# Optimization experiments

Hardware: AMD Instinct MI355X
Metric: run time of the kernel (lower is better)

The kernel has to match this reference:

```python
import jax, jax.numpy as jnp
import numpy as np

B, H, W, C, G = 64, 32, 32, 512, 1024


def setup_inputs() -> dict:
    key = jax.random.key(0)
    k1, k2, k3, k4 = jax.random.split(key, 4)
    lcf = jax.random.normal(k1, (B, H, W, C), dtype=jnp.float32)
    gbf = jax.random.normal(k2, (B, G), dtype=jnp.float32)
    # Dense(C, use_bias=False) applied to G-dim input -> kernel [G, C]
    W_proj = jax.random.normal(k3, (G, C), dtype=jnp.float32) * (G ** -0.5)
    # Dense(1, use_bias=False) applied to C-dim input -> kernel [C, 1]
    W_pc = jax.random.normal(k4, (C, 1), dtype=jnp.float32) * (C ** -0.5)
    return {"lcf": lcf, "gbf": gbf, "W_proj": W_proj, "W_pc": W_pc}


def reference(lcf, gbf, W_proj, W_pc):
    # project global feature G -> C (glf_channel != lcf_channel path)
    gbf_pj = gbf @ W_proj                              # [B, C]
    lcf_rs = lcf.reshape(-1, H * W, C)                 # [B, N, C], N = H*W
    # 'pc' (parametrised compatibility): score = (lcf + gbf) @ W_pc
    add = lcf_rs + gbf_pj[:, None, :]                  # [B, N, C]
    c = jnp.squeeze(add @ W_pc, -1)                    # [B, N]
    a = jax.nn.softmax(c, axis=1)                      # softmax over spatial locations
    # weighted sum of local features: ga[b,c] = sum_n lcf_rs[b,n,c] * a[b,n]
    ga = jnp.einsum('bnc,bn->bc', lcf_rs, a)           # [B, C]
    return ga, a.reshape(-1, H, W)
```

## Files before the change

### kernel.cpp

```cpp
#include <hip/hip_runtime.h>

#define Bb 64
#define Cc 512
#define Gg 1024
#define Nn 1024
#define NCHUNK 16
#define CHUNK (Nn / NCHUNK)

__global__ void k_wv(const float* __restrict__ Wp, const float* __restrict__ Wpc,
                     float* __restrict__ wv) {
    int wave = (blockIdx.x * blockDim.x + threadIdx.x) >> 6;
    int lane = threadIdx.x & 63;
    if (wave >= Gg) return;
    const float4* row = (const float4*)(Wp + (size_t)wave * Cc);
    const float4* pc  = (const float4*)Wpc;
    float4 a0 = row[lane * 2], a1 = row[lane * 2 + 1];
    float4 b0 = pc[lane * 2],  b1 = pc[lane * 2 + 1];
    float s = a0.x*b0.x + a0.y*b0.y + a0.z*b0.z + a0.w*b0.w
            + a1.x*b1.x + a1.y*b1.y + a1.z*b1.z + a1.w*b1.w;
    for (int off = 32; off; off >>= 1) s += __shfl_down(s, off);
    if (lane == 0) wv[wave] = s;
}

__global__ void k_bias(const float* __restrict__ gbf, const float* __restrict__ wv,
                       float* __restrict__ bias) {
    int wave = (blockIdx.x * blockDim.x + threadIdx.x) >> 6;
    int lane = threadIdx.x & 63;
    if (wave >= Bb) return;
    const float4* g4 = (const float4*)(gbf + (size_t)wave * Gg);
    const float4* w4 = (const float4*)wv;
    float s = 0.f;
    #pragma unroll
    for (int i = 0; i < 4; ++i) {
        float4 a = g4[lane * 4 + i], b = w4[lane * 4 + i];
        s += a.x*b.x + a.y*b.y + a.z*b.z + a.w*b.w;
    }
    for (int off = 32; off; off >>= 1) s += __shfl_down(s, off);
    if (lane == 0) bias[wave] = s;
}

__global__ void k_score(const float* __restrict__ lcf, const float* __restrict__ Wpc,
                        const float* __restrict__ bias, float* __restrict__ score) {
    int row  = (blockIdx.x * blockDim.x + threadIdx.x) >> 6;
    int lane = threadIdx.x & 63;
    const float4* r4 = (const float4*)(lcf + (size_t)row * Cc);
    const float4* pc = (const float4*)Wpc;
    float4 a0 = r4[lane * 2], a1 = r4[lane * 2 + 1];
    float4 b0 = pc[lane * 2], b1 = pc[lane * 2 + 1];
    float s = a0.x*b0.x + a0.y*b0.y + a0.z*b0.z + a0.w*b0.w
            + a1.x*b1.x + a1.y*b1.y + a1.z*b1.z + a1.w*b1.w;
    for (int off = 32; off; off >>= 1) s += __shfl_down(s, off);
    if (lane == 0) score[row] = s + bias[row >> 10];
}

__global__ void k_softmax(float* __restrict__ sc) {
    int b = blockIdx.x;
    int t = threadIdx.x;
    int lane = t & 63, wid = t >> 6;
    __shared__ float red[16];
    float v = sc[b * Nn + t];

    float m = v;
    for (int off = 32; off; off >>= 1) m = fmaxf(m, __shfl_down(m, off));
    if (lane == 0) red[wid] = m;
    __syncthreads();
    if (wid == 0) {
        float mm = (lane < 16) ? red[lane] : -INFINITY;
        for (int off = 32; off; off >>= 1) mm = fmaxf(mm, __shfl_down(mm, off));
        if (lane == 0) red[0] = mm;
    }
    __syncthreads();
    m = red[0];
    __syncthreads();

    float e = expf(v - m);
    float s = e;
    for (int off = 32; off; off >>= 1) s += __shfl_down(s, off);
    if (lane == 0) red[wid] = s;
    __syncthreads();
    if (wid == 0) {
        float ss = (lane < 16) ? red[lane] : 0.f;
        for (int off = 32; off; off >>= 1) ss += __shfl_down(ss, off);
        if (lane == 0) red[0] = ss;
    }
    __syncthreads();
    s = red[0];

    sc[b * Nn + t] = e / s;
}

__global__ void k_wsum(const float* __restrict__ lcf, const float* __restrict__ prob,
                       float* __restrict__ ga) {
    int b  = blockIdx.x >> 4;
    int ch = blockIdx.x & (NCHUNK - 1);
    int t  = threadIdx.x;
    __shared__ float aw[CHUNK];
    if (t < CHUNK) aw[t] = prob[b * Nn + ch * CHUNK + t];
    __syncthreads();
    const float2* base = (const float2*)(lcf + ((size_t)(b * Nn + ch * CHUNK)) * Cc);
    float2 acc = {0.f, 0.f};
    #pragma unroll 4
    for (int n = 0; n < CHUNK; ++n) {
        float2 v = base[(size_t)n * (Cc / 2) + t];
        float w = aw[n];
        acc.x += v.x * w;
        acc.y += v.y * w;
    }
    atomicAdd(&ga[b * Cc + 2 * t],     acc.x);
    atomicAdd(&ga[b * Cc + 2 * t + 1], acc.y);
}

extern "C" void kernel_launch(void* const* d_in, const int* in_sizes, int n_in,
                              void* d_out, int out_size, void* d_ws, size_t ws_size,
                              hipStream_t stream) {
    const float* lcf = (const float*)d_in[0];
    const float* gbf = (const float*)d_in[1];
    const float* Wp  = (const float*)d_in[2];
    const float* Wpc = (const float*)d_in[3];

    float* out = (float*)d_out;
    float* ga  = out;
    float* a   = out + Bb * Cc;

    float* wv   = (float*)d_ws;
    float* bias = wv + Gg;

    hipMemsetAsync(ga, 0, Bb * Cc * sizeof(float), stream);

    k_wv     <<<Gg / 4,        256, 0, stream>>>(Wp, Wpc, wv);
    k_bias   <<<Bb / 4,        256, 0, stream>>>(gbf, wv, bias);
    k_score  <<<(Bb * Nn) / 4, 256, 0, stream>>>(lcf, Wpc, bias, a);
    k_softmax<<<Bb,           1024, 0, stream>>>(a);
    k_wsum   <<<Bb * NCHUNK,   256, 0, stream>>>(lcf, a, ga);
}
```

Before: 218.7 us.

## Fuse score, online softmax and weighted sum into single pass over features

Replaces five kernels with a flash-style fused kernel that computes scores, running max/sum and rescaled weighted feature sums per 16-row partition in one read of the local features, followed by a small combine kernel that merges partitions and writes normalized attention and outputs. The global-feature projection bias is dropped since it is constant per batch and cancels in the softmax. This removes the second full pass over the large feature tensor, the memset and the atomics, at the cost of a partial-sum workspace and serial per-row shuffle reductions.

```diff
diff --git a/kernel.cpp b/kernel.cpp
--- a/kernel.cpp
+++ b/kernel.cpp
@@ -2,134 +2,122 @@
 
 #define Bb 64
 #define Cc 512
-#define Gg 1024
 #define Nn 1024
-#define NCHUNK 16
-#define CHUNK (Nn / NCHUNK)
+#define NCH 16
+#define CHUNK 64
+#define RPW 16
+#define NPART 64
 
-__global__ void k_wv(const float* __restrict__ Wp, const float* __restrict__ Wpc,
-                     float* __restrict__ wv) {
-    int wave = (blockIdx.x * blockDim.x + threadIdx.x) >> 6;
-    int lane = threadIdx.x & 63;
-    if (wave >= Gg) return;
-    const float4* row = (const float4*)(Wp + (size_t)wave * Cc);
-    const float4* pc  = (const float4*)Wpc;
-    float4 a0 = row[lane * 2], a1 = row[lane * 2 + 1];
-    float4 b0 = pc[lane * 2],  b1 = pc[lane * 2 + 1];
-    float s = a0.x*b0.x + a0.y*b0.y + a0.z*b0.z + a0.w*b0.w
-            + a1.x*b1.x + a1.y*b1.y + a1.z*b1.z + a1.w*b1.w;
-    for (int off = 32; off; off >>= 1) s += __shfl_down(s, off);
-    if (lane == 0) wv[wave] = s;
+__global__ __launch_bounds__(256) void k_flash(const float* __restrict__ lcf,
+                                               const float* __restrict__ Wpc,
+                                               float* __restrict__ c_raw,
+                                               float* __restrict__ mz,
+                                               float* __restrict__ S) {
+    int b    = blockIdx.x >> 4;
+    int ch   = blockIdx.x & 15;
+    int t    = threadIdx.x;
+    int w    = t >> 6;
+    int lane = t & 63;
+    int part = ch * 4 + w;
+
+    const float4* pc = (const float4*)Wpc;
+    float4 p0 = pc[lane * 2], p1 = pc[lane * 2 + 1];
+
+    int row0 = ch * CHUNK + w * RPW;
+    const float* base = lcf + ((size_t)b * Nn + row0) * Cc;
+
+    float m = -INFINITY, Z = 0.f;
+    float4 s0 = {0.f, 0.f, 0.f, 0.f}, s1 = {0.f, 0.f, 0.f, 0.f};
+    float myscore = 0.f;
+
+    for (int r = 0; r < RPW; ++r) {
+        const float4* row4 = (const float4*)(base + (size_t)r * Cc);
+        float4 v0 = row4[lane * 2], v1 = row4[lane * 2 + 1];
+        float d = v0.x*p0.x + v0.y*p0.y + v0.z*p0.z + v0.w*p0.w
+                + v1.x*p1.x + v1.y*p1.y + v1.z*p1.z + v1.w*p1.w;
+        #pragma unroll
+        for (int off = 32; off; off >>= 1) d += __shfl_xor(d, off);
+        if (lane == r) myscore = d;
+        float mn   = fmaxf(m, d);
+        float corr = __expf(m - mn);
+        float wgt  = __expf(d - mn);
+        Z = Z * corr + wgt;
+        s0.x = s0.x*corr + wgt*v0.x;  s0.y = s0.y*corr + wgt*v0.y;
+        s0.z = s0.z*corr + wgt*v0.z;  s0.w = s0.w*corr + wgt*v0.w;
+        s1.x = s1.x*corr + wgt*v1.x;  s1.y = s1.y*corr + wgt*v1.y;
+        s1.z = s1.z*corr + wgt*v1.z;  s1.w = s1.w*corr + wgt*v1.w;
+        m = mn;
+    }
+
+    if (lane < RPW) c_raw[(size_t)b * Nn + row0 + lane] = myscore;
+    if (lane == 0) {
+        mz[((size_t)b * NPART + part) * 2]     = m;
+        mz[((size_t)b * NPART + part) * 2 + 1] = Z;
+    }
+    float4* Sp = (float4*)(S + ((size_t)b * NPART + part) * Cc);
+    Sp[lane * 2]     = s0;
+    Sp[lane * 2 + 1] = s1;
 }
 
-__global__ void k_bias(const float* __restrict__ gbf, const float* __restrict__ wv,
-                       float* __restrict__ bias) {
-    int wave = (blockIdx.x * blockDim.x + threadIdx.x) >> 6;
-    int lane = threadIdx.x & 63;
-    if (wave >= Bb) return;
-    const float4* g4 = (const float4*)(gbf + (size_t)wave * Gg);
-    const float4* w4 = (const float4*)wv;
-    float s = 0.f;
-    #pragma unroll
-    for (int i = 0; i < 4; ++i) {
-        float4 a = g4[lane * 4 + i], b = w4[lane * 4 + i];
-        s += a.x*b.x + a.y*b.y + a.z*b.z + a.w*b.w;
-    }
-    for (int off = 32; off; off >>= 1) s += __shfl_down(s, off);
-    if (lane == 0) bias[wave] = s;
-}
-
-__global__ void k_score(const float* __restrict__ lcf, const float* __restrict__ Wpc,
-                        const float* __restrict__ bias, float* __restrict__ score) {
-    int row  = (blockIdx.x * blockDim.x + threadIdx.x) >> 6;
-    int lane = threadIdx.x & 63;
-    const float4* r4 = (const float4*)(lcf + (size_t)row * Cc);
-    const float4* pc = (const float4*)Wpc;
-    float4 a0 = r4[lane * 2], a1 = r4[lane * 2 + 1];
-    float4 b0 = pc[lane * 2], b1 = pc[lane * 2 + 1];
-    float s = a0.x*b0.x + a0.y*b0.y + a0.z*b0.z + a0.w*b0.w
-            + a1.x*b1.x + a1.y*b1.y + a1.z*b1.z + a1.w*b1.w;
-    for (int off = 32; off; off >>= 1) s += __shfl_down(s, off);
-    if (lane == 0) score[row] = s + bias[row >> 10];
-}
-
-__global__ void k_softmax(float* __restrict__ sc) {
+__global__ __launch_bounds__(256) void k_combine(const float* __restrict__ c_raw,
+                                                 const float* __restrict__ mz,
+                                                 const float* __restrict__ S,
+                                                 float* __restrict__ ga,
+                                                 float* __restrict__ a) {
     int b = blockIdx.x;
     int t = threadIdx.x;
-    int lane = t & 63, wid = t >> 6;
-    __shared__ float red[16];
-    float v = sc[b * Nn + t];
+    __shared__ float lw[NPART];
+    __shared__ float sh_M, sh_invZ;
 
-    float m = v;
-    for (int off = 32; off; off >>= 1) m = fmaxf(m, __shfl_down(m, off));
-    if (lane == 0) red[wid] = m;
-    __syncthreads();
-    if (wid == 0) {
-        float mm = (lane < 16) ? red[lane] : -INFINITY;
-        for (int off = 32; off; off >>= 1) mm = fmaxf(mm, __shfl_down(mm, off));
-        if (lane == 0) red[0] = mm;
+    if (t < NPART) {
+        float mi = mz[((size_t)b * NPART + t) * 2];
+        float zi = mz[((size_t)b * NPART + t) * 2 + 1];
+        float M = mi;
+        #pragma unroll
+        for (int off = 32; off; off >>= 1) M = fmaxf(M, __shfl_xor(M, off));
+        float wi = __expf(mi - M);
+        float zc = zi * wi;
+        #pragma unroll
+        for (int off = 32; off; off >>= 1) zc += __shfl_xor(zc, off);
+        lw[t] = wi;
+        if (t == 0) { sh_M = M; sh_invZ = 1.f / zc; }
     }
     __syncthreads();
-    m = red[0];
-    __syncthreads();
+    float M = sh_M, invZ = sh_invZ;
 
-    float e = expf(v - m);
-    float s = e;
-    for (int off = 32; off; off >>= 1) s += __shfl_down(s, off);
-    if (lane == 0) red[wid] = s;
-    __syncthreads();
-    if (wid == 0) {
-        float ss = (lane < 16) ? red[lane] : 0.f;
-        for (int off = 32; off; off >>= 1) ss += __shfl_down(ss, off);
-        if (lane == 0) red[0] = ss;
-    }
-    __syncthreads();
-    s = red[0];
-
-    sc[b * Nn + t] = e / s;
-}
-
-__global__ void k_wsum(const float* __restrict__ lcf, const float* __restrict__ prob,
-                       float* __restrict__ ga) {
-    int b  = blockIdx.x >> 4;
-    int ch = blockIdx.x & (NCHUNK - 1);
-    int t  = threadIdx.x;
-    __shared__ float aw[CHUNK];
-    if (t < CHUNK) aw[t] = prob[b * Nn + ch * CHUNK + t];
-    __syncthreads();
-    const float2* base = (const float2*)(lcf + ((size_t)(b * Nn + ch * CHUNK)) * Cc);
+    const float2* Sp = (const float2*)(S + (size_t)b * NPART * Cc);
     float2 acc = {0.f, 0.f};
     #pragma unroll 4
-    for (int n = 0; n < CHUNK; ++n) {
-        float2 v = base[(size_t)n * (Cc / 2) + t];
-        float w = aw[n];
-        acc.x += v.x * w;
-        acc.y += v.y * w;
+    for (int i = 0; i < NPART; ++i) {
+        float wgt = lw[i];
+        float2 v  = Sp[(size_t)i * (Cc / 2) + t];
+        acc.x += wgt * v.x;
+        acc.y += wgt * v.y;
     }
-    atomicAdd(&ga[b * Cc + 2 * t],     acc.x);
-    atomicAdd(&ga[b * Cc + 2 * t + 1], acc.y);
+    ga[(size_t)b * Cc + 2 * t]     = acc.x * invZ;
+    ga[(size_t)b * Cc + 2 * t + 1] = acc.y * invZ;
+
+    #pragma unroll
+    for (int k = 0; k < 4; ++k) {
+        int n = t + k * 256;
+        a[(size_t)b * Nn + n] = __expf(c_raw[(size_t)b * Nn + n] - M) * invZ;
+    }
 }
 
 extern "C" void kernel_launch(void* const* d_in, const int* in_sizes, int n_in,
                               void* d_out, int out_size, void* d_ws, size_t ws_size,
                               hipStream_t stream) {
     const float* lcf = (const float*)d_in[0];
-    const float* gbf = (const float*)d_in[1];
-    const float* Wp  = (const float*)d_in[2];
     const float* Wpc = (const float*)d_in[3];
 
     float* out = (float*)d_out;
     float* ga  = out;
     float* a   = out + Bb * Cc;
 
-    float* wv   = (float*)d_ws;
-    float* bias = wv + Gg;
+    float* c_raw = (float*)d_ws;
+    float* mzbuf = c_raw + (size_t)Bb * Nn;
+    float* Sbuf  = mzbuf + (size_t)Bb * NPART * 2;
 
-    hipMemsetAsync(ga, 0, Bb * Cc * sizeof(float), stream);
-
-    k_wv     <<<Gg / 4,        256, 0, stream>>>(Wp, Wpc, wv);
-    k_bias   <<<Bb / 4,        256, 0, stream>>>(gbf, wv, bias);
-    k_score  <<<(Bb * Nn) / 4, 256, 0, stream>>>(lcf, Wpc, bias, a);
-    k_softmax<<<Bb,           1024, 0, stream>>>(a);
-    k_wsum   <<<Bb * NCHUNK,   256, 0, stream>>>(lcf, a, ga);
+    k_flash  <<<Bb * NCH, 256, 0, stream>>>(lcf, Wpc, c_raw, mzbuf, Sbuf);
+    k_combine<<<Bb,       256, 0, stream>>>(c_raw, mzbuf, Sbuf, ga, a);
 }
```

Measured after the change: 202.9 us. -7.2%, faster.
